# Optimization experiments

Measured on AMD Instinct MI355X. Metric: run time of the kernel, lower is better.

The kernel has to match this reference:

```python
import jax, jax.numpy as jnp
import numpy as np

D_MODEL, D_INNER, D_STATE, D_CONV, DT_RANK = 512, 1024, 64, 4, 32
B, L = 2, 1000
EPS = 1e-5


def _rmsnorm(x, w):
    return x * jax.lax.rsqrt(jnp.mean(x * x, axis=-1, keepdims=True) + EPS) * w


def _causal_dwconv(x, w, b):
    # x: (B, L, Di); w: (Di, K) depthwise causal conv, output length L
    xT = jnp.transpose(x, (0, 2, 1))  # (B, Di, L)
    y = jax.lax.conv_general_dilated(
        xT, w[:, None, :], window_strides=(1,), padding=[(D_CONV - 1, 0)],
        dimension_numbers=('NCH', 'OIH', 'NCH'), feature_group_count=D_INNER)
    return jnp.transpose(y + b[None, :, None], (0, 2, 1))


def _selective_scan(u, dt, A, Bm, Cm):
    # u, dt: (B, L, Di); A: (Di, N); Bm, Cm: (B, L, N)
    def step(h, inp):
        dt_t, B_t, C_t, u_t = inp
        dA = jnp.exp(dt_t[..., None] * A)                       # (B, Di, N)
        h = dA * h + (dt_t * u_t)[..., None] * B_t[:, None, :]  # state update
        y = jnp.einsum('bdn,bn->bd', h, C_t)
        return h, y
    xs = (jnp.swapaxes(dt, 0, 1), jnp.swapaxes(Bm, 0, 1),
          jnp.swapaxes(Cm, 0, 1), jnp.swapaxes(u, 0, 1))
    h0 = jnp.zeros((u.shape[0], D_INNER, D_STATE), u.dtype)
    _, ys = jax.lax.scan(step, h0, xs)
    return jnp.swapaxes(ys, 0, 1)  # (B, L, Di)


def _mamba_layer(x, norm_w, in_proj, conv_w, conv_b, x_proj, dt_w, dt_b, A_log, Dp, out_proj):
    # mamba-ssm Block with fused_add_norm=False, n_layer=1:
    # residual = x; h = mixer(rmsnorm(x)); block output pair merges to h + x
    h = _rmsnorm(x, norm_w)
    xz = jnp.einsum('bld,ed->ble', h, in_proj)        # (B, L, 2*Di)
    xc, z = jnp.split(xz, 2, axis=-1)
    xc = jax.nn.silu(_causal_dwconv(xc, conv_w, conv_b))
    x_dbl = jnp.einsum('bld,ed->ble', xc, x_proj)     # (B, L, dt_rank + 2N)
    dt, Bm, Cm = jnp.split(x_dbl, [DT_RANK, DT_RANK + D_STATE], axis=-1)
    dt = jax.nn.softplus(jnp.einsum('blr,dr->bld', dt, dt_w) + dt_b)
    A = -jnp.exp(A_log)
    y = _selective_scan(xc, dt, A, Bm, Cm)
    y = (y + xc * Dp) * jax.nn.silu(z)
    return jnp.einsum('bld,ed->ble', y, out_proj) + x


def _forward(x,
             f_norm_w, f_in_proj, f_conv_w, f_conv_b, f_x_proj, f_dt_w, f_dt_b, f_A_log, f_D, f_out_proj,
             b_norm_w, b_in_proj, b_conv_w, b_conv_b, b_x_proj, b_dt_w, b_dt_b, b_A_log, b_D, b_out_proj):
    res_f = _mamba_layer(x, f_norm_w, f_in_proj, f_conv_w, f_conv_b, f_x_proj,
                         f_dt_w, f_dt_b, f_A_log, f_D, f_out_proj)
    res_b = _mamba_layer(jnp.flip(x, 1), b_norm_w, b_in_proj, b_conv_w, b_conv_b,
                         b_x_proj, b_dt_w, b_dt_b, b_A_log, b_D, b_out_proj)
    return res_f + jnp.flip(res_b, 1)  # bidirectional_merging='add'


def setup_inputs() -> dict:
    key = jax.random.key(0)
    ks = iter(jax.random.split(key, 32))
    def nrm(shape, s=0.02):
        return jax.random.normal(next(ks), shape, jnp.float32) * s
    inp = {'x': jax.random.normal(next(ks), (B, L, D_MODEL), jnp.float32)}
    for p in ('f', 'b'):
        inp[p + '_norm_w'] = jnp.ones((D_MODEL,), jnp.float32)
        inp[p + '_in_proj'] = nrm((2 * D_INNER, D_MODEL))
        inp[p + '_conv_w'] = nrm((D_INNER, D_CONV), 0.1)
        inp[p + '_conv_b'] = nrm((D_INNER,), 0.1)
        inp[p + '_x_proj'] = nrm((DT_RANK + 2 * D_STATE, D_INNER))
        inp[p + '_dt_w'] = nrm((D_INNER, DT_RANK), 0.1)
        inp[p + '_dt_b'] = jnp.full((D_INNER,), float(np.log(np.expm1(0.01))), jnp.float32)
        inp[p + '_A_log'] = jnp.log(jnp.tile(jnp.arange(1, D_STATE + 1, dtype=jnp.float32), (D_INNER, 1)))
        inp[p + '_D'] = jnp.ones((D_INNER,), jnp.float32)
        inp[p + '_out_proj'] = nrm((D_MODEL, D_INNER))
    return inp


def reference(x,
              f_norm_w, f_in_proj, f_conv_w, f_conv_b, f_x_proj, f_dt_w, f_dt_b, f_A_log, f_D, f_out_proj,
              b_norm_w, b_in_proj, b_conv_w, b_conv_b, b_x_proj, b_dt_w, b_dt_b, b_A_log, b_D, b_out_proj):
    return _forward(x,
                    f_norm_w, f_in_proj, f_conv_w, f_conv_b, f_x_proj, f_dt_w, f_dt_b, f_A_log, f_D, f_out_proj,
                    b_norm_w, b_in_proj, b_conv_w, b_conv_b, b_x_proj, b_dt_w, b_dt_b, b_A_log, b_D, b_out_proj)
```

## Files before the change

kernel.cpp:

```cpp
#include <hip/hip_runtime.h>
#include <hip/hip_bf16.h>
#include <math.h>

#define DM   512
#define DI   1024
#define NS   64
#define RDT  32
#define BB   2
#define LL   1000
#define MROWS (BB*LL)

typedef __attribute__((ext_vector_type(8))) short bf16x8;
typedef __attribute__((ext_vector_type(4))) float f32x4;

__device__ __forceinline__ unsigned short f2bf(float f) {
    unsigned u = __builtin_bit_cast(unsigned, f);
    u = (u + 0x7FFF + ((u >> 16) & 1)) >> 16;
    return (unsigned short)u;
}

__device__ __forceinline__ float bcast_lane(float v, int lane) {
    return __builtin_bit_cast(float,
        __builtin_amdgcn_readlane(__builtin_bit_cast(int, v), lane));
}

__global__ __launch_bounds__(256)
void rmsnorm_k(const float* __restrict__ x,
               const float* __restrict__ nw0, const float* __restrict__ nw1,
               unsigned short* __restrict__ xnb0, unsigned short* __restrict__ xnb1) {
    int row = blockIdx.x;
    int tid = threadIdx.x;
    const float* xr = x + (size_t)row * DM;
    float2 v = *(const float2*)(xr + tid * 2);
    float ss = v.x * v.x + v.y * v.y;
    #pragma unroll
    for (int off = 32; off; off >>= 1) ss += __shfl_xor(ss, off, 64);
    __shared__ float red[4];
    if ((tid & 63) == 0) red[tid >> 6] = ss;
    __syncthreads();
    float tot = red[0] + red[1] + red[2] + red[3];
    float scale = rsqrtf(tot / (float)DM + 1e-5f);
    float2 w0 = *(const float2*)(nw0 + tid * 2);
    float2 w1 = *(const float2*)(nw1 + tid * 2);
    short2 o0, o1;
    o0.x = (short)f2bf(v.x * scale * w0.x);
    o0.y = (short)f2bf(v.y * scale * w0.y);
    o1.x = (short)f2bf(v.x * scale * w1.x);
    o1.y = (short)f2bf(v.y * scale * w1.y);
    *(short2*)(xnb0 + (size_t)row * DM + tid * 2) = o0;
    *(short2*)(xnb1 + (size_t)row * DM + tid * 2) = o1;
}

__global__ __launch_bounds__(256)
void cvt2_k(const float* __restrict__ in0, const float* __restrict__ in1,
            unsigned short* __restrict__ out0, unsigned short* __restrict__ out1,
            int n4) {
    int idx = blockIdx.x * 256 + threadIdx.x;
    if (idx >= n4) return;
    const float* in = blockIdx.y ? in1 : in0;
    unsigned short* out = blockIdx.y ? out1 : out0;
    float4 v = *(const float4*)(in + (size_t)idx * 4);
    short4 o;
    o.x = (short)f2bf(v.x); o.y = (short)f2bf(v.y);
    o.z = (short)f2bf(v.z); o.w = (short)f2bf(v.w);
    *(short4*)(out + (size_t)idx * 4) = o;
}

__global__ __launch_bounds__(256, 2)
void gemm1_mfma(const unsigned short* __restrict__ xnb0,
                const unsigned short* __restrict__ xnb1,
                const unsigned short* __restrict__ wib0,
                const unsigned short* __restrict__ wib1,
                float* __restrict__ xz0, float* __restrict__ xz1)
{
    __shared__ __align__(16) unsigned short As[128 * 40];
    __shared__ __align__(16) unsigned short Bs[128 * 40];
    int dir = blockIdx.z;
    const unsigned short* A = dir ? xnb1 : xnb0;
    const unsigned short* W = dir ? wib1 : wib0;
    float* C = dir ? xz1 : xz0;
    int n0 = blockIdx.x * 128, m0 = blockIdx.y * 128;
    int tid = threadIdx.x;
    int wv = tid >> 6, lane = tid & 63;
    int wr = wv >> 1, wc = wv & 1;
    int fl = lane & 15, kg = lane >> 4;

    f32x4 acc[4][4];
    #pragma unroll
    for (int i = 0; i < 4; i++)
        #pragma unroll
        for (int j = 0; j < 4; j++) acc[i][j] = (f32x4){0.f, 0.f, 0.f, 0.f};

    int sr = tid >> 2, cg = tid & 3;
    for (int k0 = 0; k0 < 512; k0 += 32) {
        #pragma unroll
        for (int i = 0; i < 2; i++) {
            int row = sr + i * 64;
            int m = m0 + row;
            float4 av = make_float4(0.f, 0.f, 0.f, 0.f);
            if (m < MROWS) {
                int rs = m;
                if (dir) { int b = m / LL, t = m % LL; rs = b * LL + (LL - 1 - t); }
                av = *(const float4*)(A + (size_t)rs * 512 + k0 + cg * 8);
            }
            *(float4*)(&As[row * 40 + cg * 8]) = av;
            float4 wv4 = *(const float4*)(W + (size_t)(n0 + row) * 512 + k0 + cg * 8);
            *(float4*)(&Bs[row * 40 + cg * 8]) = wv4;
        }
        __syncthreads();
        bf16x8 af[4], bf[4];
        #pragma unroll
        for (int fr = 0; fr < 4; fr++)
            af[fr] = *(const bf16x8*)(&As[(wr * 64 + fr * 16 + fl) * 40 + kg * 8]);
        #pragma unroll
        for (int fc = 0; fc < 4; fc++)
            bf[fc] = *(const bf16x8*)(&Bs[(wc * 64 + fc * 16 + fl) * 40 + kg * 8]);
        #pragma unroll
        for (int fr = 0; fr < 4; fr++)
            #pragma unroll
            for (int fc = 0; fc < 4; fc++)
                acc[fr][fc] = __builtin_amdgcn_mfma_f32_16x16x32_bf16(
                    af[fr], bf[fc], acc[fr][fc], 0, 0, 0);
        __syncthreads();
    }
    #pragma unroll
    for (int fr = 0; fr < 4; fr++)
        #pragma unroll
        for (int fc = 0; fc < 4; fc++)
            #pragma unroll
            for (int j = 0; j < 4; j++) {
                int m = m0 + wr * 64 + fr * 16 + kg * 4 + j;
                if (m < MROWS) {
                    int n = n0 + wc * 64 + fc * 16 + fl;
                    C[(size_t)m * 2048 + n] = acc[fr][fc][j];
                }
            }
}

__global__ __launch_bounds__(256, 2)
void gemm_out_mfma(const unsigned short* __restrict__ ygb0,
                   const unsigned short* __restrict__ ygb1,
                   const unsigned short* __restrict__ wob0,
                   const unsigned short* __restrict__ wob1,
                   float* __restrict__ partial)
{
    __shared__ __align__(16) unsigned short As[128 * 40];
    __shared__ __align__(16) unsigned short Bs[128 * 40];
    int dir = blockIdx.z;
    const unsigned short* A = dir ? ygb1 : ygb0;
    const unsigned short* W = dir ? wob1 : wob0;
    float* P = partial + (size_t)dir * MROWS * 512;
    int n0 = blockIdx.x * 128, m0 = blockIdx.y * 128;
    int tid = threadIdx.x;
    int wv = tid >> 6, lane = tid & 63;
    int wr = wv >> 1, wc = wv & 1;
    int fl = lane & 15, kg = lane >> 4;

    f32x4 acc[4][4];
    #pragma unroll
    for (int i = 0; i < 4; i++)
        #pragma unroll
        for (int j = 0; j < 4; j++) acc[i][j] = (f32x4){0.f, 0.f, 0.f, 0.f};

    int sr = tid >> 2, cg = tid & 3;
    for (int k0 = 0; k0 < 1024; k0 += 32) {
        #pragma unroll
        for (int i = 0; i < 2; i++) {
            int row = sr + i * 64;
            int m = m0 + row;
            float4 av = make_float4(0.f, 0.f, 0.f, 0.f);
            if (m < MROWS)
                av = *(const float4*)(A + (size_t)m * 1024 + k0 + cg * 8);
            *(float4*)(&As[row * 40 + cg * 8]) = av;
            float4 wv4 = *(const float4*)(W + (size_t)(n0 + row) * 1024 + k0 + cg * 8);
            *(float4*)(&Bs[row * 40 + cg * 8]) = wv4;
        }
        __syncthreads();
        bf16x8 af[4], bf[4];
        #pragma unroll
        for (int fr = 0; fr < 4; fr++)
            af[fr] = *(const bf16x8*)(&As[(wr * 64 + fr * 16 + fl) * 40 + kg * 8]);
        #pragma unroll
        for (int fc = 0; fc < 4; fc++)
            bf[fc] = *(const bf16x8*)(&Bs[(wc * 64 + fc * 16 + fl) * 40 + kg * 8]);
        #pragma unroll
        for (int fr = 0; fr < 4; fr++)
            #pragma unroll
            for (int fc = 0; fc < 4; fc++)
                acc[fr][fc] = __builtin_amdgcn_mfma_f32_16x16x32_bf16(
                    af[fr], bf[fc], acc[fr][fc], 0, 0, 0);
        __syncthreads();
    }
    #pragma unroll
    for (int fr = 0; fr < 4; fr++)
        #pragma unroll
        for (int fc = 0; fc < 4; fc++)
            #pragma unroll
            for (int j = 0; j < 4; j++) {
                int m = m0 + wr * 64 + fr * 16 + kg * 4 + j;
                if (m < MROWS) {
                    int n = n0 + wc * 64 + fc * 16 + fl;
                    P[(size_t)m * 512 + n] = acc[fr][fc][j];
                }
            }
}

__global__ __launch_bounds__(256)
void reduce_out_k(const float* __restrict__ x, const float* __restrict__ partial,
                  float* __restrict__ out)
{
    int idx = blockIdx.x * 256 + threadIdx.x;
    if (idx >= MROWS * 128) return;
    int m = idx >> 7, q = idx & 127;
    int b = m / LL, t = m % LL;
    int fm = b * LL + (LL - 1 - t);
    const float* p0 = partial;
    const float* p1 = partial + (size_t)MROWS * 512;
    float4 xv = *(const float4*)(x  + (size_t)m  * 512 + q * 4);
    float4 a  = *(const float4*)(p0 + (size_t)m  * 512 + q * 4);
    float4 c  = *(const float4*)(p1 + (size_t)fm * 512 + q * 4);
    float4 o;
    o.x = 2.f * xv.x + a.x + c.x;
    o.y = 2.f * xv.y + a.y + c.y;
    o.z = 2.f * xv.z + a.z + c.z;
    o.w = 2.f * xv.w + a.w + c.w;
    *(float4*)(out + (size_t)m * 512 + q * 4) = o;
}

__global__ __launch_bounds__(256)
void conv_silu_k(const float* __restrict__ xz0, const float* __restrict__ xz1,
                 const float* __restrict__ cw0, const float* __restrict__ cw1,
                 const float* __restrict__ cb0, const float* __restrict__ cb1,
                 float* __restrict__ xcT0, float* __restrict__ xcT1,
                 unsigned short* __restrict__ xcb0, unsigned short* __restrict__ xcb1)
{
    __shared__ float Ls[64 * 65];
    int dirb = blockIdx.z;
    int dir = dirb >> 1, b = dirb & 1;
    int d0 = blockIdx.x * 64, t0 = blockIdx.y * 64;
    int tid = threadIdx.x;
    int dl = tid & 63, tg = tid >> 6;

    const float* in = (dir ? xz1 : xz0) + (size_t)b * LL * 2048;
    const float* cw = dir ? cw1 : cw0;
    const float* cb = dir ? cb1 : cb0;
    float*      xcT = dir ? xcT1 : xcT0;
    unsigned short* xcb = dir ? xcb1 : xcb0;

    float4 w4 = ((const float4*)cw)[d0 + dl];
    float bias = cb[d0 + dl];

    int ts = t0 + tg * 16;
    float x3 = 0.f, x2 = 0.f, x1 = 0.f;
    if (ts - 3 >= 0 && ts - 3 < LL) x3 = in[(size_t)(ts - 3) * 2048 + d0 + dl];
    if (ts - 2 >= 0 && ts - 2 < LL) x2 = in[(size_t)(ts - 2) * 2048 + d0 + dl];
    if (ts - 1 >= 0 && ts - 1 < LL) x1 = in[(size_t)(ts - 1) * 2048 + d0 + dl];

    #pragma unroll
    for (int i = 0; i < 16; i++) {
        int t = ts + i;
        float x0v = (t < LL) ? in[(size_t)t * 2048 + d0 + dl] : 0.f;
        float a = bias + x3 * w4.x + x2 * w4.y + x1 * w4.z + x0v * w4.w;
        float s = a / (1.f + __expf(-a));
        Ls[dl * 65 + tg * 16 + i] = s;
        if (t < LL)
            xcb[((size_t)(b * LL + t)) * 1024 + d0 + dl] = f2bf(s);
        x3 = x2; x2 = x1; x1 = x0v;
    }
    __syncthreads();
    int tl = tid & 63, dg = tid >> 6;
    #pragma unroll
    for (int i = 0; i < 16; i++) {
        int dd = dg * 16 + i;
        int t = t0 + tl;
        if (t < LL)
            xcT[((size_t)(b * 1024) + d0 + dd) * LL + t] = Ls[dd * 65 + tl];
    }
}

__global__ __launch_bounds__(256, 2)
void gemm_xp_mfma(const unsigned short* __restrict__ xcb0,
                  const unsigned short* __restrict__ xcb1,
                  const unsigned short* __restrict__ xpb0,
                  const unsigned short* __restrict__ xpb1,
                  float* __restrict__ xd0, float* __restrict__ xd1,
                  float* __restrict__ bct)
{
    __shared__ __align__(16) unsigned short As[64 * 40];
    __shared__ __align__(16) unsigned short Ws[160 * 40];
    int dirb = blockIdx.y;
    int dir = dirb >> 1, b = dirb & 1;
    const unsigned short* A = (dir ? xcb1 : xcb0) + (size_t)b * LL * 1024;
    const unsigned short* W = dir ? xpb1 : xpb0;
    float* xd = (dir ? xd1 : xd0) + (size_t)b * LL * 32;
    float* bc = bct + (size_t)dirb * 128 * LL;
    int m0 = blockIdx.x * 64;
    int tid = threadIdx.x;
    int wv = tid >> 6, lane = tid & 63;
    int fl = lane & 15, kg = lane >> 4;

    f32x4 acc[10];
    #pragma unroll
    for (int f = 0; f < 10; f++) acc[f] = (f32x4){0.f, 0.f, 0.f, 0.f};

    int sr = tid >> 2, cg = tid & 3;
    for (int k0 = 0; k0 < 1024; k0 += 32) {
        {
            int t = m0 + sr;
            float4 av = make_float4(0.f, 0.f, 0.f, 0.f);
            if (t < LL)
                av = *(const float4*)(A + (size_t)t * 1024 + k0 + cg * 8);
            *(float4*)(&As[sr * 40 + cg * 8]) = av;
        }
        #pragma unroll
        for (int it = 0; it < 3; it++) {
            int row = sr + it * 64;
            if (row < 160) {
                float4 wv4 = *(const float4*)(W + (size_t)row * 1024 + k0 + cg * 8);
                *(float4*)(&Ws[row * 40 + cg * 8]) = wv4;
            }
        }
        __syncthreads();
        bf16x8 af = *(const bf16x8*)(&As[(wv * 16 + fl) * 40 + kg * 8]);
        #pragma unroll
        for (int f = 0; f < 10; f++) {
            bf16x8 bf = *(const bf16x8*)(&Ws[(f * 16 + fl) * 40 + kg * 8]);
            acc[f] = __builtin_amdgcn_mfma_f32_16x16x32_bf16(af, bf, acc[f], 0, 0, 0);
        }
        __syncthreads();
    }

    #pragma unroll
    for (int f = 0; f < 10; f++) {
        int n = f * 16 + fl;
        #pragma unroll
        for (int j = 0; j < 4; j++) {
            int t = m0 + wv * 16 + kg * 4 + j;
            if (t >= LL) continue;
            if (f < 2) xd[(size_t)t * 32 + n] = acc[f][j];
            else       bc[(size_t)(n - 32) * LL + t] = acc[f][j];
        }
    }
}

__global__ __launch_bounds__(256)
void gemm_dt_k(const float* __restrict__ xd0, const float* __restrict__ xd1,
               const float* __restrict__ w0, const float* __restrict__ w1,
               const float* __restrict__ bb0, const float* __restrict__ bb1,
               float* __restrict__ dtT0, float* __restrict__ dtT1)
{
    __shared__ float As[64 * 33];
    __shared__ float Ws[32 * 68];
    __shared__ float T[64 * 67];
    int dirb = blockIdx.z;
    int dir = dirb >> 1, b = dirb & 1;
    const float* xd = (dir ? xd1 : xd0) + (size_t)b * LL * 32;
    const float* W  = dir ? w1 : w0;
    const float* bi = dir ? bb1 : bb0;
    float*      dtT = (dir ? dtT1 : dtT0) + (size_t)b * 1024 * LL;
    int n0 = blockIdx.x * 64, t0 = blockIdx.y * 64;
    int tid = threadIdx.x;
    int tx = tid & 15, ty = tid >> 4;

    #pragma unroll
    for (int i = 0; i < 2; i++) {
        int j = tid + 256 * i;
        int row = j >> 3, q = j & 7;
        float4 v = make_float4(0.f, 0.f, 0.f, 0.f);
        if (t0 + row < LL)
            v = *(const float4*)(xd + (size_t)(t0 + row) * 32 + q * 4);
        As[row * 33 + q * 4 + 0] = v.x;
        As[row * 33 + q * 4 + 1] = v.y;
        As[row * 33 + q * 4 + 2] = v.z;
        As[row * 33 + q * 4 + 3] = v.w;
        float4 wv = *(const float4*)(W + (size_t)(n0 + row) * 32 + q * 4);
        Ws[(q * 4 + 0) * 68 + row] = wv.x;
        Ws[(q * 4 + 1) * 68 + row] = wv.y;
        Ws[(q * 4 + 2) * 68 + row] = wv.z;
        Ws[(q * 4 + 3) * 68 + row] = wv.w;
    }
    __syncthreads();

    float acc[4][4] = {};
    #pragma unroll 8
    for (int k = 0; k < 32; k++) {
        float4 w = *(const float4*)(Ws + k * 68 + tx * 4);
        float wvv[4] = {w.x, w.y, w.z, w.w};
        float av[4];
        #pragma unroll
        for (int i = 0; i < 4; i++) av[i] = As[(ty * 4 + i) * 33 + k];
        #pragma unroll
        for (int i = 0; i < 4; i++)
            #pragma unroll
            for (int j = 0; j < 4; j++)
                acc[i][j] = fmaf(av[i], wvv[j], acc[i][j]);
    }
    __syncthreads();

    #pragma unroll
    for (int i = 0; i < 4; i++) {
        #pragma unroll
        for (int j = 0; j < 4; j++) {
            int n = tx * 4 + j;
            float v = acc[i][j] + bi[n0 + n];
            v = (v > 20.f) ? v : log1pf(__expf(v));
            T[n * 67 + ty * 4 + i] = v;
        }
    }
    __syncthreads();

    int tl = tid & 63, ng = tid >> 6;
    #pragma unroll
    for (int i = 0; i < 16; i++) {
        int nl = ng * 16 + i;
        int t = t0 + tl;
        if (t < LL)
            dtT[(size_t)(n0 + nl) * LL + t] = T[nl * 67 + tl];
    }
}

__global__ __launch_bounds__(256)
void scan_k(float* __restrict__ dtT0, float* __restrict__ dtT1,
            const float* __restrict__ ucT0, const float* __restrict__ ucT1,
            const float* __restrict__ bct,
            const float* __restrict__ Al0, const float* __restrict__ Al1,
            const float* __restrict__ Dc0, const float* __restrict__ Dc1)
{
    __shared__ float Bs[64 * 34];
    __shared__ float Cs[64 * 34];
    __shared__ float Pt[4][16 * 66];
    int dirb = blockIdx.y;
    int dir = dirb >> 1, b = dirb & 1;
    int wid = threadIdx.x >> 6, lane = threadIdx.x & 63;
    int d = blockIdx.x * 4 + wid;
    float* Pw = Pt[wid];

    float*       dtT = (dir ? dtT1 : dtT0);
    const float* ucT = (dir ? ucT1 : ucT0);
    const float* Al  = dir ? Al1 : Al0;
    const float* Dc  = dir ? Dc1 : Dc0;

    float a  = -__expf(Al[d * 64 + lane]) * 1.44269504f;
    float Dp = Dc[d];
    float h  = 0.f;
    size_t chan = ((size_t)(b * 1024 + d)) * LL;
    const float* Bg = bct + (size_t)dirb * 128 * LL;

    int srow = threadIdx.x >> 2;
    int scol = (threadIdx.x & 3) * 8;
    int tl16 = lane & 15, qq = lane >> 4;
    const float* Prow = Pw + tl16 * 66 + qq * 16;

    float4 rb0, rb1, rc0, rc1;
    float dta = 0.f, ua = 0.f;
    {
        const float* Bp = Bg + (size_t)srow * LL + scol;
        const float* Cp = Bg + (size_t)(srow + 64) * LL + scol;
        rb0 = *(const float4*)(Bp);     rb1 = *(const float4*)(Bp + 4);
        rc0 = *(const float4*)(Cp);     rc1 = *(const float4*)(Cp + 4);
        if (lane < 32) {
            dta = dtT[chan + lane];
            ua  = ucT[chan + lane];
        }
    }

    for (int t0 = 0; t0 < LL; t0 += 32) {
        int rem = min(32, LL - t0);
        __syncthreads();
        *(float4*)(&Bs[srow * 34 + scol])     = rb0;
        *(float4*)(&Bs[srow * 34 + scol + 4]) = rb1;
        *(float4*)(&Cs[srow * 34 + scol])     = rc0;
        *(float4*)(&Cs[srow * 34 + scol + 4]) = rc1;
        float dcur = dta, ucur = ua;
        float wsc  = dcur * ucur;
        __syncthreads();

        if (t0 + 32 < LL) {
            const float* Bp = Bg + (size_t)srow * LL + (t0 + 32) + scol;
            const float* Cp = Bg + (size_t)(srow + 64) * LL + (t0 + 32) + scol;
            rb0 = *(const float4*)(Bp);     rb1 = *(const float4*)(Bp + 4);
            rc0 = *(const float4*)(Cp);     rc1 = *(const float4*)(Cp + 4);
            if (lane < min(32, LL - t0 - 32)) {
                dta = dtT[chan + t0 + 32 + lane];
                ua  = ucT[chan + t0 + 32 + lane];
            }
        }

        for (int sec = 0; sec < 2; sec++) {
            int sbase = sec * 16;
            int steps = rem - sbase;
            if (steps <= 0) break;
            if (steps > 16) steps = 16;
            if (steps < 16) {
                for (int i = steps; i < 16; i++) Pw[i * 66 + lane] = 0.f;
            }
            int ngr = (steps + 7) >> 3;
            for (int g = 0; g < ngr; g++) {
                int tb = sbase + g * 8;
                float4 B0 = *(const float4*)(&Bs[lane * 34 + tb]);
                float4 B1 = *(const float4*)(&Bs[lane * 34 + tb + 4]);
                float4 C0 = *(const float4*)(&Cs[lane * 34 + tb]);
                float4 C1 = *(const float4*)(&Cs[lane * 34 + tb + 4]);
                #pragma unroll
                for (int i = 0; i < 8; i++) {
                    float dtv = bcast_lane(dcur, tb + i);
                    float w   = bcast_lane(wsc,  tb + i);
                    float dA  = exp2f(dtv * a);
                    float Bn  = (i < 4) ? B0[i] : B1[i - 4];
                    float Cn  = (i < 4) ? C0[i] : C1[i - 4];
                    h = fmaf(dA, h, w * Bn);
                    Pw[(g * 8 + i) * 66 + lane] = h * Cn;
                }
            }
            float s = 0.f;
            #pragma unroll
            for (int j = 0; j < 8; j++) {
                float2 v = *(const float2*)(Prow + j * 2);
                s += v.x + v.y;
            }
#if __has_builtin(__builtin_amdgcn_permlane32_swap)
            {
                unsigned aa = __builtin_bit_cast(unsigned, s);
                auto r = __builtin_amdgcn_permlane32_swap(aa, aa, false, false);
                s = __builtin_bit_cast(float, (unsigned)r[0]) +
                    __builtin_bit_cast(float, (unsigned)r[1]);
            }
#else
            s += __shfl_xor(s, 32, 64);
#endif
#if __has_builtin(__builtin_amdgcn_permlane16_swap)
            {
                unsigned aa = __builtin_bit_cast(unsigned, s);
                auto r = __builtin_amdgcn_permlane16_swap(aa, aa, false, false);
                s = __builtin_bit_cast(float, (unsigned)r[0]) +
                    __builtin_bit_cast(float, (unsigned)r[1]);
            }
#else
            s += __shfl_xor(s, 16, 64);
#endif
            float uf = __shfl(ucur, sbase + tl16, 64);
            s = fmaf(uf, Dp, s);
            if (lane < steps)
                dtT[chan + t0 + sbase + lane] = s;
        }
    }
}

__global__ __launch_bounds__(256)
void gate_k(const float* __restrict__ yT0, const float* __restrict__ yT1,
            const float* __restrict__ xz0, const float* __restrict__ xz1,
            unsigned short* __restrict__ yg0, unsigned short* __restrict__ yg1)
{
    __shared__ float Ls[64 * 65];
    int dirb = blockIdx.z;
    int dir = dirb >> 1, b = dirb & 1;
    int d0 = blockIdx.x * 64, t0 = blockIdx.y * 64;
    int tid = threadIdx.x;
    const float* yT = (dir ? yT1 : yT0) + (size_t)b * 1024 * LL;
    const float* xz = (dir ? xz1 : xz0) + (size_t)b * LL * 2048;
    unsigned short* yg = dir ? yg1 : yg0;

    int tl = tid & 63, dg = tid >> 6;
    #pragma unroll
    for (int i = 0; i < 16; i++) {
        int dd = dg * 16 + i;
        int t = t0 + tl;
        float v = (t < LL) ? yT[(size_t)(d0 + dd) * LL + t] : 0.f;
        Ls[dd * 65 + tl] = v;
    }
    __syncthreads();
    int dcol = tid & 63, tg = tid >> 6;
    #pragma unroll
    for (int i = 0; i < 16; i++) {
        int t = t0 + tg * 16 + i;
        if (t >= LL) continue;
        float z = xz[(size_t)t * 2048 + 1024 + d0 + dcol];
        float y = Ls[dcol * 65 + tg * 16 + i];
        float s = z / (1.f + __expf(-z));
        yg[((size_t)(b * LL + t)) * 1024 + d0 + dcol] = f2bf(y * s);
    }
}

extern "C" void kernel_launch(void* const* d_in, const int* in_sizes, int n_in,
                              void* d_out, int out_size, void* d_ws, size_t ws_size,
                              hipStream_t stream) {
    const float* x = (const float*)d_in[0];
    const float* P[2][10];
    for (int dir = 0; dir < 2; dir++)
        for (int i = 0; i < 10; i++)
            P[dir][i] = (const float*)d_in[1 + dir * 10 + i];

    float* ws = (float*)d_ws;
    float* xz0   = ws;
    float* xz1   = ws + 4096000;
    float* xcT0  = ws + 8192000;
    float* xcT1  = ws + 10240000;
    float* dtT0  = ws + 12288000;
    float* dtT1  = ws + 14336000;
    float* xdbl0 = ws + 16384000;
    float* xdbl1 = ws + 16448000;
    unsigned short* xnb0 = (unsigned short*)(ws + 17024000);
    unsigned short* xnb1 = (unsigned short*)(ws + 17280000);
    unsigned short* wib0 = (unsigned short*)(ws + 14336000);
    unsigned short* wib1 = (unsigned short*)(ws + 14860288);
    unsigned short* xcb0 = (unsigned short*)(ws + 12288000);
    unsigned short* xcb1 = (unsigned short*)(ws + 13312000);
    unsigned short* xpb0 = (unsigned short*)(ws + 17024000);
    unsigned short* xpb1 = (unsigned short*)(ws + 17280000);
    unsigned short* ygb0 = (unsigned short*)xcT0;
    unsigned short* ygb1 = (unsigned short*)xcT1;
    unsigned short* wob0 = (unsigned short*)dtT0;
    unsigned short* wob1 = (unsigned short*)(dtT0 + 262144);
    float* partial = xz0;
    float* bct = (float*)d_out;
    float* out = (float*)d_out;

    rmsnorm_k<<<MROWS, 256, 0, stream>>>(x, P[0][0], P[1][0], xnb0, xnb1);

    cvt2_k<<<dim3(1024, 2), 256, 0, stream>>>(P[0][1], P[1][1], wib0, wib1, 262144);

    gemm1_mfma<<<dim3(16, 16, 2), 256, 0, stream>>>(
        xnb0, xnb1, wib0, wib1, xz0, xz1);

    cvt2_k<<<dim3(160, 2), 256, 0, stream>>>(P[0][4], P[1][4], xpb0, xpb1, 40960);

    conv_silu_k<<<dim3(16, 16, 4), 256, 0, stream>>>(
        xz0, xz1, P[0][2], P[1][2], P[0][3], P[1][3], xcT0, xcT1, xcb0, xcb1);

    gemm_xp_mfma<<<dim3(16, 4), 256, 0, stream>>>(
        xcb0, xcb1, xpb0, xpb1, xdbl0, xdbl1, bct);

    gemm_dt_k<<<dim3(16, 16, 4), 256, 0, stream>>>(
        xdbl0, xdbl1, P[0][5], P[1][5], P[0][6], P[1][6], dtT0, dtT1);

    scan_k<<<dim3(256, 4), 256, 0, stream>>>(
        dtT0, dtT1, xcT0, xcT1, bct,
        P[0][7], P[1][7], P[0][8], P[1][8]);

    gate_k<<<dim3(16, 16, 4), 256, 0, stream>>>(
        dtT0, dtT1, xz0, xz1, ygb0, ygb1);

    cvt2_k<<<dim3(512, 2), 256, 0, stream>>>(P[0][9], P[1][9], wob0, wob1, 131072);

    gemm_out_mfma<<<dim3(4, 16, 2), 256, 0, stream>>>(
        ygb0, ygb1, wob0, wob1, partial);

    reduce_out_k<<<1000, 256, 0, stream>>>(x, partial, out);
}
```

Baseline: 296.7 us.

## Store xz and conv output in bf16 and fuse dt projection into x_proj GEMM

The in_proj GEMM now writes xz as bf16 instead of fp32, and the transposed conv output used by the scan is stored as bf16. This halves the traffic for these large intermediates. The separate dt GEMM kernel is removed: the x_proj MFMA kernel stages the dt-rank slice in shared memory as bf16 and computes dt = softplus(W_dt·x + b) with MFMA, writing the transposed dt directly. This saves a launch and a round-trip through xdbl, at the cost of bf16 rounding on xz, u and the dt input, and a serial loop of 64 small MFMAs per block.

```diff
diff --git a/kernel.cpp b/kernel.cpp
--- a/kernel.cpp
+++ b/kernel.cpp
@@ -18,7 +18,10 @@
     u = (u + 0x7FFF + ((u >> 16) & 1)) >> 16;
     return (unsigned short)u;
 }
-
+__device__ __forceinline__ float bf2f(unsigned short h) {
+    unsigned u = (unsigned)h << 16;
+    return __builtin_bit_cast(float, u);
+}
 __device__ __forceinline__ float bcast_lane(float v, int lane) {
     return __builtin_bit_cast(float,
         __builtin_amdgcn_readlane(__builtin_bit_cast(int, v), lane));
@@ -66,19 +69,40 @@
     *(short4*)(out + (size_t)idx * 4) = o;
 }
 
+__global__ __launch_bounds__(256)
+void cvt_xpdw_k(const float* __restrict__ xp0, const float* __restrict__ xp1,
+                const float* __restrict__ dw0, const float* __restrict__ dw1,
+                unsigned short* __restrict__ oxp0, unsigned short* __restrict__ oxp1,
+                unsigned short* __restrict__ odw0, unsigned short* __restrict__ odw1)
+{
+    int y = blockIdx.y;
+    const float* in; unsigned short* out; int n4;
+    if (y == 0)      { in = xp0; out = oxp0; n4 = 40960; }
+    else if (y == 1) { in = xp1; out = oxp1; n4 = 40960; }
+    else if (y == 2) { in = dw0; out = odw0; n4 = 8192; }
+    else             { in = dw1; out = odw1; n4 = 8192; }
+    int idx = blockIdx.x * 256 + threadIdx.x;
+    if (idx >= n4) return;
+    float4 v = *(const float4*)(in + (size_t)idx * 4);
+    short4 o;
+    o.x = (short)f2bf(v.x); o.y = (short)f2bf(v.y);
+    o.z = (short)f2bf(v.z); o.w = (short)f2bf(v.w);
+    *(short4*)(out + (size_t)idx * 4) = o;
+}
+
 __global__ __launch_bounds__(256, 2)
 void gemm1_mfma(const unsigned short* __restrict__ xnb0,
                 const unsigned short* __restrict__ xnb1,
                 const unsigned short* __restrict__ wib0,
                 const unsigned short* __restrict__ wib1,
-                float* __restrict__ xz0, float* __restrict__ xz1)
+                unsigned short* __restrict__ xzb0, unsigned short* __restrict__ xzb1)
 {
     __shared__ __align__(16) unsigned short As[128 * 40];
     __shared__ __align__(16) unsigned short Bs[128 * 40];
     int dir = blockIdx.z;
     const unsigned short* A = dir ? xnb1 : xnb0;
     const unsigned short* W = dir ? wib1 : wib0;
-    float* C = dir ? xz1 : xz0;
+    unsigned short* C = dir ? xzb1 : xzb0;
     int n0 = blockIdx.x * 128, m0 = blockIdx.y * 128;
     int tid = threadIdx.x;
     int wv = tid >> 6, lane = tid & 63;
@@ -132,7 +156,7 @@
                 int m = m0 + wr * 64 + fr * 16 + kg * 4 + j;
                 if (m < MROWS) {
                     int n = n0 + wc * 64 + fc * 16 + fl;
-                    C[(size_t)m * 2048 + n] = acc[fr][fc][j];
+                    C[(size_t)m * 2048 + n] = f2bf(acc[fr][fc][j]);
                 }
             }
 }
@@ -228,10 +252,11 @@
 }
 
 __global__ __launch_bounds__(256)
-void conv_silu_k(const float* __restrict__ xz0, const float* __restrict__ xz1,
+void conv_silu_k(const unsigned short* __restrict__ xzb0,
+                 const unsigned short* __restrict__ xzb1,
                  const float* __restrict__ cw0, const float* __restrict__ cw1,
                  const float* __restrict__ cb0, const float* __restrict__ cb1,
-                 float* __restrict__ xcT0, float* __restrict__ xcT1,
+                 unsigned short* __restrict__ ucb0, unsigned short* __restrict__ ucb1,
                  unsigned short* __restrict__ xcb0, unsigned short* __restrict__ xcb1)
 {
     __shared__ float Ls[64 * 65];
@@ -241,10 +266,10 @@
     int tid = threadIdx.x;
     int dl = tid & 63, tg = tid >> 6;
 
-    const float* in = (dir ? xz1 : xz0) + (size_t)b * LL * 2048;
+    const unsigned short* in = (dir ? xzb1 : xzb0) + (size_t)b * LL * 2048;
     const float* cw = dir ? cw1 : cw0;
     const float* cb = dir ? cb1 : cb0;
-    float*      xcT = dir ? xcT1 : xcT0;
+    unsigned short* ucb = dir ? ucb1 : ucb0;
     unsigned short* xcb = dir ? xcb1 : xcb0;
 
     float4 w4 = ((const float4*)cw)[d0 + dl];
@@ -252,14 +277,14 @@
 
     int ts = t0 + tg * 16;
     float x3 = 0.f, x2 = 0.f, x1 = 0.f;
-    if (ts - 3 >= 0 && ts - 3 < LL) x3 = in[(size_t)(ts - 3) * 2048 + d0 + dl];
-    if (ts - 2 >= 0 && ts - 2 < LL) x2 = in[(size_t)(ts - 2) * 2048 + d0 + dl];
-    if (ts - 1 >= 0 && ts - 1 < LL) x1 = in[(size_t)(ts - 1) * 2048 + d0 + dl];
+    if (ts - 3 >= 0 && ts - 3 < LL) x3 = bf2f(in[(size_t)(ts - 3) * 2048 + d0 + dl]);
+    if (ts - 2 >= 0 && ts - 2 < LL) x2 = bf2f(in[(size_t)(ts - 2) * 2048 + d0 + dl]);
+    if (ts - 1 >= 0 && ts - 1 < LL) x1 = bf2f(in[(size_t)(ts - 1) * 2048 + d0 + dl]);
 
     #pragma unroll
     for (int i = 0; i < 16; i++) {
         int t = ts + i;
-        float x0v = (t < LL) ? in[(size_t)t * 2048 + d0 + dl] : 0.f;
+        float x0v = (t < LL) ? bf2f(in[(size_t)t * 2048 + d0 + dl]) : 0.f;
         float a = bias + x3 * w4.x + x2 * w4.y + x1 * w4.z + x0v * w4.w;
         float s = a / (1.f + __expf(-a));
         Ls[dl * 65 + tg * 16 + i] = s;
@@ -274,7 +299,7 @@
         int dd = dg * 16 + i;
         int t = t0 + tl;
         if (t < LL)
-            xcT[((size_t)(b * 1024) + d0 + dd) * LL + t] = Ls[dd * 65 + tl];
+            ucb[((size_t)(b * 1024) + d0 + dd) * LL + t] = f2bf(Ls[dd * 65 + tl]);
     }
 }
 
@@ -283,17 +308,23 @@
                   const unsigned short* __restrict__ xcb1,
                   const unsigned short* __restrict__ xpb0,
                   const unsigned short* __restrict__ xpb1,
-                  float* __restrict__ xd0, float* __restrict__ xd1,
+                  const unsigned short* __restrict__ dwb0,
+                  const unsigned short* __restrict__ dwb1,
+                  const float* __restrict__ db0, const float* __restrict__ db1,
+                  float* __restrict__ dtT0, float* __restrict__ dtT1,
                   float* __restrict__ bct)
 {
     __shared__ __align__(16) unsigned short As[64 * 40];
     __shared__ __align__(16) unsigned short Ws[160 * 40];
+    __shared__ __align__(16) unsigned short Ds[64 * 40];
     int dirb = blockIdx.y;
     int dir = dirb >> 1, b = dirb & 1;
-    const unsigned short* A = (dir ? xcb1 : xcb0) + (size_t)b * LL * 1024;
-    const unsigned short* W = dir ? xpb1 : xpb0;
-    float* xd = (dir ? xd1 : xd0) + (size_t)b * LL * 32;
-    float* bc = bct + (size_t)dirb * 128 * LL;
+    const unsigned short* A  = (dir ? xcb1 : xcb0) + (size_t)b * LL * 1024;
+    const unsigned short* W  = dir ? xpb1 : xpb0;
+    const unsigned short* DW = dir ? dwb1 : dwb0;
+    const float* DB = dir ? db1 : db0;
+    float* dtT = (dir ? dtT1 : dtT0) + (size_t)b * 1024 * LL;
+    float* bc  = bct + (size_t)dirb * 128 * LL;
     int m0 = blockIdx.x * 64;
     int tid = threadIdx.x;
     int wv = tid >> 6, lane = tid & 63;
@@ -331,97 +362,50 @@
     }
 
     #pragma unroll
-    for (int f = 0; f < 10; f++) {
+    for (int f = 2; f < 10; f++) {
         int n = f * 16 + fl;
         #pragma unroll
         for (int j = 0; j < 4; j++) {
             int t = m0 + wv * 16 + kg * 4 + j;
-            if (t >= LL) continue;
-            if (f < 2) xd[(size_t)t * 32 + n] = acc[f][j];
-            else       bc[(size_t)(n - 32) * LL + t] = acc[f][j];
-        }
-    }
-}
-
-__global__ __launch_bounds__(256)
-void gemm_dt_k(const float* __restrict__ xd0, const float* __restrict__ xd1,
-               const float* __restrict__ w0, const float* __restrict__ w1,
-               const float* __restrict__ bb0, const float* __restrict__ bb1,
-               float* __restrict__ dtT0, float* __restrict__ dtT1)
-{
-    __shared__ float As[64 * 33];
-    __shared__ float Ws[32 * 68];
-    __shared__ float T[64 * 67];
-    int dirb = blockIdx.z;
-    int dir = dirb >> 1, b = dirb & 1;
-    const float* xd = (dir ? xd1 : xd0) + (size_t)b * LL * 32;
-    const float* W  = dir ? w1 : w0;
-    const float* bi = dir ? bb1 : bb0;
-    float*      dtT = (dir ? dtT1 : dtT0) + (size_t)b * 1024 * LL;
-    int n0 = blockIdx.x * 64, t0 = blockIdx.y * 64;
-    int tid = threadIdx.x;
-    int tx = tid & 15, ty = tid >> 4;
-
-    #pragma unroll
-    for (int i = 0; i < 2; i++) {
-        int j = tid + 256 * i;
-        int row = j >> 3, q = j & 7;
-        float4 v = make_float4(0.f, 0.f, 0.f, 0.f);
-        if (t0 + row < LL)
-            v = *(const float4*)(xd + (size_t)(t0 + row) * 32 + q * 4);
-        As[row * 33 + q * 4 + 0] = v.x;
-        As[row * 33 + q * 4 + 1] = v.y;
-        As[row * 33 + q * 4 + 2] = v.z;
-        As[row * 33 + q * 4 + 3] = v.w;
-        float4 wv = *(const float4*)(W + (size_t)(n0 + row) * 32 + q * 4);
-        Ws[(q * 4 + 0) * 68 + row] = wv.x;
-        Ws[(q * 4 + 1) * 68 + row] = wv.y;
-        Ws[(q * 4 + 2) * 68 + row] = wv.z;
-        Ws[(q * 4 + 3) * 68 + row] = wv.w;
-    }
+            if (t < LL) bc[(size_t)(n - 32) * LL + t] = acc[f][j];
+        }
+    }
+
+    #pragma unroll
+    for (int f = 0; f < 2; f++)
+        #pragma unroll
+        for (int j = 0; j < 4; j++)
+            Ds[(wv * 16 + kg * 4 + j) * 40 + f * 16 + fl] = f2bf(acc[f][j]);
     __syncthreads();
 
-    float acc[4][4] = {};
-    #pragma unroll 8
-    for (int k = 0; k < 32; k++) {
-        float4 w = *(const float4*)(Ws + k * 68 + tx * 4);
-        float wvv[4] = {w.x, w.y, w.z, w.w};
-        float av[4];
-        #pragma unroll
-        for (int i = 0; i < 4; i++) av[i] = As[(ty * 4 + i) * 33 + k];
-        #pragma unroll
-        for (int i = 0; i < 4; i++)
+    bf16x8 af2 = *(const bf16x8*)(&Ds[(wv * 16 + fl) * 40 + kg * 8]);
+    for (int nb = 0; nb < 64; nb++) {
+        bf16x8 bfr = *(const bf16x8*)(DW + (size_t)(nb * 16 + fl) * 32 + kg * 8);
+        f32x4 ad = __builtin_amdgcn_mfma_f32_16x16x32_bf16(
+            af2, bfr, (f32x4){0.f, 0.f, 0.f, 0.f}, 0, 0, 0);
+        float bias = DB[nb * 16 + fl];
+        float4 st;
+        #pragma unroll
+        for (int j = 0; j < 4; j++) {
+            float v = ad[j] + bias;
+            st[j] = (v > 20.f) ? v : log1pf(__expf(v));
+        }
+        int tb = m0 + wv * 16 + kg * 4;
+        float* drow = dtT + (size_t)(nb * 16 + fl) * LL + tb;
+        if (tb + 3 < LL) {
+            *(float4*)drow = st;
+        } else {
             #pragma unroll
             for (int j = 0; j < 4; j++)
-                acc[i][j] = fmaf(av[i], wvv[j], acc[i][j]);
-    }
-    __syncthreads();
-
-    #pragma unroll
-    for (int i = 0; i < 4; i++) {
-        #pragma unroll
-        for (int j = 0; j < 4; j++) {
-            int n = tx * 4 + j;
-            float v = acc[i][j] + bi[n0 + n];
-            v = (v > 20.f) ? v : log1pf(__expf(v));
-            T[n * 67 + ty * 4 + i] = v;
-        }
-    }
-    __syncthreads();
-
-    int tl = tid & 63, ng = tid >> 6;
-    #pragma unroll
-    for (int i = 0; i < 16; i++) {
-        int nl = ng * 16 + i;
-        int t = t0 + tl;
-        if (t < LL)
-            dtT[(size_t)(n0 + nl) * LL + t] = T[nl * 67 + tl];
+                if (tb + j < LL) drow[j] = st[j];
+        }
     }
 }
 
 __global__ __launch_bounds__(256)
 void scan_k(float* __restrict__ dtT0, float* __restrict__ dtT1,
-            const float* __restrict__ ucT0, const float* __restrict__ ucT1,
+            const unsigned short* __restrict__ ucT0,
+            const unsigned short* __restrict__ ucT1,
             const float* __restrict__ bct,
             const float* __restrict__ Al0, const float* __restrict__ Al1,
             const float* __restrict__ Dc0, const float* __restrict__ Dc1)
@@ -436,7 +420,7 @@
     float* Pw = Pt[wid];
 
     float*       dtT = (dir ? dtT1 : dtT0);
-    const float* ucT = (dir ? ucT1 : ucT0);
+    const unsigned short* ucT = (dir ? ucT1 : ucT0);
     const float* Al  = dir ? Al1 : Al0;
     const float* Dc  = dir ? Dc1 : Dc0;
 
@@ -460,7 +444,7 @@
         rc0 = *(const float4*)(Cp);     rc1 = *(const float4*)(Cp + 4);
         if (lane < 32) {
             dta = dtT[chan + lane];
-            ua  = ucT[chan + lane];
+            ua  = bf2f(ucT[chan + lane]);
         }
     }
 
@@ -482,7 +466,7 @@
             rc0 = *(const float4*)(Cp);     rc1 = *(const float4*)(Cp + 4);
             if (lane < min(32, LL - t0 - 32)) {
                 dta = dtT[chan + t0 + 32 + lane];
-                ua  = ucT[chan + t0 + 32 + lane];
+                ua  = bf2f(ucT[chan + t0 + 32 + lane]);
             }
         }
 
@@ -548,7 +532,8 @@
 
 __global__ __launch_bounds__(256)
 void gate_k(const float* __restrict__ yT0, const float* __restrict__ yT1,
-            const float* __restrict__ xz0, const float* __restrict__ xz1,
+            const unsigned short* __restrict__ xzb0,
+            const unsigned short* __restrict__ xzb1,
             unsigned short* __restrict__ yg0, unsigned short* __restrict__ yg1)
 {
     __shared__ float Ls[64 * 65];
@@ -557,7 +542,7 @@
     int d0 = blockIdx.x * 64, t0 = blockIdx.y * 64;
     int tid = threadIdx.x;
     const float* yT = (dir ? yT1 : yT0) + (size_t)b * 1024 * LL;
-    const float* xz = (dir ? xz1 : xz0) + (size_t)b * LL * 2048;
+    const unsigned short* xz = (dir ? xzb1 : xzb0) + (size_t)b * LL * 2048;
     unsigned short* yg = dir ? yg1 : yg0;
 
     int tl = tid & 63, dg = tid >> 6;
@@ -574,7 +559,7 @@
     for (int i = 0; i < 16; i++) {
         int t = t0 + tg * 16 + i;
         if (t >= LL) continue;
-        float z = xz[(size_t)t * 2048 + 1024 + d0 + dcol];
+        float z = bf2f(xz[(size_t)t * 2048 + 1024 + d0 + dcol]);
         float y = Ls[dcol * 65 + tg * 16 + i];
         float s = z / (1.f + __expf(-z));
         yg[((size_t)(b * LL + t)) * 1024 + d0 + dcol] = f2bf(y * s);
@@ -591,27 +576,27 @@
             P[dir][i] = (const float*)d_in[1 + dir * 10 + i];
 
     float* ws = (float*)d_ws;
-    float* xz0   = ws;
-    float* xz1   = ws + 4096000;
-    float* xcT0  = ws + 8192000;
-    float* xcT1  = ws + 10240000;
-    float* dtT0  = ws + 12288000;
-    float* dtT1  = ws + 14336000;
-    float* xdbl0 = ws + 16384000;
-    float* xdbl1 = ws + 16448000;
-    unsigned short* xnb0 = (unsigned short*)(ws + 17024000);
-    unsigned short* xnb1 = (unsigned short*)(ws + 17280000);
-    unsigned short* wib0 = (unsigned short*)(ws + 14336000);
-    unsigned short* wib1 = (unsigned short*)(ws + 14860288);
-    unsigned short* xcb0 = (unsigned short*)(ws + 12288000);
-    unsigned short* xcb1 = (unsigned short*)(ws + 13312000);
-    unsigned short* xpb0 = (unsigned short*)(ws + 17024000);
-    unsigned short* xpb1 = (unsigned short*)(ws + 17280000);
-    unsigned short* ygb0 = (unsigned short*)xcT0;
-    unsigned short* ygb1 = (unsigned short*)xcT1;
-    unsigned short* wob0 = (unsigned short*)dtT0;
-    unsigned short* wob1 = (unsigned short*)(dtT0 + 262144);
-    float* partial = xz0;
+    unsigned short* xzb0 = (unsigned short*)(ws);
+    unsigned short* xzb1 = (unsigned short*)(ws + 2048000);
+    unsigned short* ucb0 = (unsigned short*)(ws + 4096000);
+    unsigned short* ucb1 = (unsigned short*)(ws + 5120000);
+    float* dtT0 = ws + 6144000;
+    float* dtT1 = ws + 8192000;
+    unsigned short* xcb0 = (unsigned short*)(ws + 10240000);
+    unsigned short* xcb1 = (unsigned short*)(ws + 11264000);
+    unsigned short* xnb0 = (unsigned short*)(ws + 12288000);
+    unsigned short* xnb1 = (unsigned short*)(ws + 12800000);
+    unsigned short* wib0 = (unsigned short*)(ws + 13312000);
+    unsigned short* wib1 = (unsigned short*)(ws + 13836288);
+    unsigned short* xpb0 = (unsigned short*)(ws + 14360576);
+    unsigned short* xpb1 = (unsigned short*)(ws + 14442496);
+    unsigned short* dwb0 = (unsigned short*)(ws + 14524416);
+    unsigned short* dwb1 = (unsigned short*)(ws + 14540800);
+    unsigned short* ygb0 = xcb0;
+    unsigned short* ygb1 = xcb1;
+    unsigned short* wob0 = wib0;
+    unsigned short* wob1 = wib1;
+    float* partial = dtT0;
     float* bct = (float*)d_out;
     float* out = (float*)d_out;
 
@@ -620,25 +605,25 @@
     cvt2_k<<<dim3(1024, 2), 256, 0, stream>>>(P[0][1], P[1][1], wib0, wib1, 262144);
 
     gemm1_mfma<<<dim3(16, 16, 2), 256, 0, stream>>>(
-        xnb0, xnb1, wib0, wib1, xz0, xz1);
-
-    cvt2_k<<<dim3(160, 2), 256, 0, stream>>>(P[0][4], P[1][4], xpb0, xpb1, 40960);
+        xnb0, xnb1, wib0, wib1, xzb0, xzb1);
+
+    cvt_xpdw_k<<<dim3(160, 4), 256, 0, stream>>>(
+        P[0][4], P[1][4], P[0][5], P[1][5], xpb0, xpb1, dwb0, dwb1);
 
     conv_silu_k<<<dim3(16, 16, 4), 256, 0, stream>>>(
-        xz0, xz1, P[0][2], P[1][2], P[0][3], P[1][3], xcT0, xcT1, xcb0, xcb1);
+        xzb0, xzb1, P[0][2], P[1][2], P[0][3], P[1][3],
+        ucb0, ucb1, xcb0, xcb1);
 
     gemm_xp_mfma<<<dim3(16, 4), 256, 0, stream>>>(
-        xcb0, xcb1, xpb0, xpb1, xdbl0, xdbl1, bct);
-
-    gemm_dt_k<<<dim3(16, 16, 4), 256, 0, stream>>>(
-        xdbl0, xdbl1, P[0][5], P[1][5], P[0][6], P[1][6], dtT0, dtT1);
+        xcb0, xcb1, xpb0, xpb1, dwb0, dwb1, P[0][6], P[1][6],
+        dtT0, dtT1, bct);
 
     scan_k<<<dim3(256, 4), 256, 0, stream>>>(
-        dtT0, dtT1, xcT0, xcT1, bct,
+        dtT0, dtT1, ucb0, ucb1, bct,
         P[0][7], P[1][7], P[0][8], P[1][8]);
 
     gate_k<<<dim3(16, 16, 4), 256, 0, stream>>>(
-        dtT0, dtT1, xz0, xz1, ygb0, ygb1);
+        dtT0, dtT1, xzb0, xzb1, ygb0, ygb1);
 
     cvt2_k<<<dim3(512, 2), 256, 0, stream>>>(P[0][9], P[1][9], wob0, wob1, 131072);
 
```

Measured after the change: 366.1 us. 1.23x slower.
